# Kernel optimization log

Hardware: AMD Instinct MI355X
Metric: run time of the kernel (lower is better)

## Reference

```python
import jax, jax.numpy as jnp
import numpy as np

WIN_SIZE = 11
SIGMA = 1.5
DATA_RANGE = 1.0
K1, K2 = 0.01, 0.03


def _gaussian_1d(size=WIN_SIZE, sigma=SIGMA):
    coords = np.arange(size, dtype=np.float32) - (size - 1) / 2.0
    g = np.exp(-(coords ** 2) / (2.0 * sigma ** 2))
    g = g / g.sum()
    return jnp.asarray(g, dtype=jnp.float32)


def _gaussian_blur(x):
    # Separable depthwise Gaussian blur, VALID padding (matches pytorch-msssim).
    B, C, H, W = x.shape
    g = _gaussian_1d().astype(x.dtype)
    kh = jnp.tile(g.reshape(1, 1, WIN_SIZE, 1), (C, 1, 1, 1))
    kw = jnp.tile(g.reshape(1, 1, 1, WIN_SIZE), (C, 1, 1, 1))
    dn = ('NCHW', 'OIHW', 'NCHW')
    x = jax.lax.conv_general_dilated(x, kh, (1, 1), 'VALID',
                                     dimension_numbers=dn, feature_group_count=C)
    x = jax.lax.conv_general_dilated(x, kw, (1, 1), 'VALID',
                                     dimension_numbers=dn, feature_group_count=C)
    return x


def _ssim(X, Y):
    C1 = (K1 * DATA_RANGE) ** 2
    C2 = (K2 * DATA_RANGE) ** 2

    mu1 = _gaussian_blur(X)
    mu2 = _gaussian_blur(Y)
    mu1_sq = mu1 * mu1
    mu2_sq = mu2 * mu2
    mu1_mu2 = mu1 * mu2

    sigma1_sq = _gaussian_blur(X * X) - mu1_sq
    sigma2_sq = _gaussian_blur(Y * Y) - mu2_sq
    sigma12 = _gaussian_blur(X * Y) - mu1_mu2

    cs_map = (2.0 * sigma12 + C2) / (sigma1_sq + sigma2_sq + C2)
    ssim_map = ((2.0 * mu1_mu2 + C1) / (mu1_sq + mu2_sq + C1)) * cs_map

    ssim_per_channel = ssim_map.mean(axis=(2, 3))  # [B, C]
    return ssim_per_channel


def setup_inputs() -> dict:
    key = jax.random.key(0)
    k1, k2 = jax.random.split(key)
    predictions = jax.random.uniform(k1, (32, 3, 512, 512), dtype=jnp.float32)
    labels = jax.random.uniform(k2, (32, 3, 512, 512), dtype=jnp.float32)
    return {"predictions": predictions, "labels": labels}


def reference(predictions, labels):
    ssim_per_channel = _ssim(predictions, labels)
    # nonnegative_ssim=True -> relu; size_average=True -> scalar mean
    ssim_val = jax.nn.relu(ssim_per_channel).mean()
    return 1.0 - ssim_val
```

## Files before the change

### kernel.cpp

```cpp
#include <hip/hip_runtime.h>


#define IMG 512
#define OUT_DIM 502
#define WIN 11
#define BH 32
#define NPHASE (BH + WIN - 1)
#define NPLANES 96

template<int PH>
__device__ __forceinline__ void phase_step(int base, int r0, int c0, int cbase,
                                           const float* __restrict__ Xp,
                                           const float* __restrict__ Yp,
                                           float (&a)[5][2][WIN], float& local) {
    constexpr float G[WIN] = {0.00102838f, 0.00759875f, 0.03600077f, 0.10936071f,
                              0.21300553f, 0.26601172f, 0.21300553f, 0.10936071f,
                              0.03600077f, 0.00759875f, 0.00102838f};
    const int p = base + PH;
    if (p >= NPHASE) return;
    const int rr = min(r0 + p, IMG - 1);
    const float* px = Xp + rr * IMG + cbase;
    const float* py = Yp + rr * IMG + cbase;

    float x[12], y[12];
    #pragma unroll
    for (int i = 0; i < 6; ++i) {
        const float2 xv = *(const float2*)(px + 2 * i);
        const float2 yv = *(const float2*)(py + 2 * i);
        x[2 * i] = xv.x; x[2 * i + 1] = xv.y;
        y[2 * i] = yv.x; y[2 * i + 1] = yv.y;
    }
    float xx[12], yy[12], xy[12];
    #pragma unroll
    for (int i = 0; i < 12; ++i) {
        xx[i] = x[i] * x[i];
        yy[i] = y[i] * y[i];
        xy[i] = x[i] * y[i];
    }

    float h[5][2];
    #pragma unroll
    for (int c = 0; c < 2; ++c) {
        float h0 = 0.f, h1 = 0.f, h2 = 0.f, h3 = 0.f, h4 = 0.f;
        #pragma unroll
        for (int k = 0; k < WIN; ++k) {
            h0 = fmaf(G[k], x[k + c], h0);
            h1 = fmaf(G[k], y[k + c], h1);
            h2 = fmaf(G[k], xx[k + c], h2);
            h3 = fmaf(G[k], yy[k + c], h3);
            h4 = fmaf(G[k], xy[k + c], h4);
        }
        h[0][c] = h0; h[1][c] = h1; h[2][c] = h2; h[3][c] = h3; h[4][c] = h4;
    }

    #pragma unroll
    for (int d = 0; d < WIN; ++d) {
        constexpr int ds = PH;
        const int s = (ds - d + 2 * WIN) % WIN;
        const float w = G[d];
        #pragma unroll
        for (int m = 0; m < 5; ++m)
            #pragma unroll
            for (int c = 0; c < 2; ++c)
                a[m][c][s] = (d == 0) ? (w * h[m][c]) : fmaf(w, h[m][c], a[m][c][s]);
    }

    if (p >= WIN - 1) {
        const int o = r0 + p - (WIN - 1);
        if (o < OUT_DIM && c0 < OUT_DIM) {
            constexpr int se = (PH + 1) % WIN;
            const float C1 = 0.0001f, C2 = 0.0009f;
            #pragma unroll
            for (int c = 0; c < 2; ++c) {
                const float m1 = a[0][c][se], m2 = a[1][c][se];
                const float m1sq = m1 * m1, m2sq = m2 * m2, m12 = m1 * m2;
                const float s1  = a[2][c][se] - m1sq;
                const float s2  = a[3][c][se] - m2sq;
                const float s12 = a[4][c][se] - m12;
                const float num = (2.f * m12 + C1) * (2.f * s12 + C2);
                const float den = (m1sq + m2sq + C1) * (s1 + s2 + C2);
                local += num * __builtin_amdgcn_rcpf(den);
            }
        }
    }
}

__global__ __launch_bounds__(256, 2) void ssim_stream(const float* __restrict__ X,
                                                      const float* __restrict__ Y,
                                                      float* __restrict__ planeSums) {
    const int tid = threadIdx.x;
    const int r0 = blockIdx.x * BH;
    const int plane = blockIdx.y;
    const size_t pbase = (size_t)plane * IMG * IMG;
    const float* Xp = X + pbase;
    const float* Yp = Y + pbase;
    const int c0 = tid << 1;
    const int cbase = min(c0, IMG - 12);

    float a[5][2][WIN];
    float local = 0.f;

    for (int base = 0; base < 44; base += WIN) {
        phase_step<0>(base, r0, c0, cbase, Xp, Yp, a, local);
        phase_step<1>(base, r0, c0, cbase, Xp, Yp, a, local);
        phase_step<2>(base, r0, c0, cbase, Xp, Yp, a, local);
        phase_step<3>(base, r0, c0, cbase, Xp, Yp, a, local);
        phase_step<4>(base, r0, c0, cbase, Xp, Yp, a, local);
        phase_step<5>(base, r0, c0, cbase, Xp, Yp, a, local);
        phase_step<6>(base, r0, c0, cbase, Xp, Yp, a, local);
        phase_step<7>(base, r0, c0, cbase, Xp, Yp, a, local);
        phase_step<8>(base, r0, c0, cbase, Xp, Yp, a, local);
        phase_step<9>(base, r0, c0, cbase, Xp, Yp, a, local);
        phase_step<10>(base, r0, c0, cbase, Xp, Yp, a, local);
    }

    #pragma unroll
    for (int off = 32; off > 0; off >>= 1)
        local += __shfl_down(local, off, 64);
    __shared__ float red[4];
    if ((tid & 63) == 0) red[tid >> 6] = local;
    __syncthreads();
    if (tid == 0)
        atomicAdd(&planeSums[plane], (red[0] + red[1]) + (red[2] + red[3]));
}

__global__ __launch_bounds__(128) void ssim_finalize(const float* __restrict__ planeSums,
                                                     float* __restrict__ out) {
    const int tid = threadIdx.x;
    float v = 0.f;
    if (tid < NPLANES) {
        const float m = planeSums[tid] * (1.0f / (float)(OUT_DIM * OUT_DIM));
        v = fmaxf(m, 0.f);
    }
    #pragma unroll
    for (int off = 32; off > 0; off >>= 1)
        v += __shfl_down(v, off, 64);
    __shared__ float red[2];
    if ((tid & 63) == 0) red[tid >> 6] = v;
    __syncthreads();
    if (tid == 0) out[0] = 1.0f - (red[0] + red[1]) * (1.0f / (float)NPLANES);
}

extern "C" void kernel_launch(void* const* d_in, const int* in_sizes, int n_in,
                              void* d_out, int out_size, void* d_ws, size_t ws_size,
                              hipStream_t stream) {
    const float* X = (const float*)d_in[0];
    const float* Y = (const float*)d_in[1];
    float* out = (float*)d_out;
    float* ws  = (float*)d_ws;

    hipMemsetAsync(ws, 0, NPLANES * sizeof(float), stream);

    dim3 grid((OUT_DIM + BH - 1) / BH, NPLANES);
    ssim_stream<<<grid, 256, 0, stream>>>(X, Y, ws);
    ssim_finalize<<<1, 128, 0, stream>>>(ws, out);
}
```

Baseline: 346.5 us.

## Compute one output column per thread with parity-shifted weights for higher occupancy

```diff
diff --git a/kernel.cpp b/kernel.cpp
--- a/kernel.cpp
+++ b/kernel.cpp
@@ -9,10 +9,11 @@
 #define NPLANES 96
 
 template<int PH>
-__device__ __forceinline__ void phase_step(int base, int r0, int c0, int cbase,
+__device__ __forceinline__ void phase_step(int base, int r0, int c, int cbase,
                                            const float* __restrict__ Xp,
                                            const float* __restrict__ Yp,
-                                           float (&a)[5][2][WIN], float& local) {
+                                           const float (&W)[12],
+                                           float (&a)[5][WIN], float& local) {
     constexpr float G[WIN] = {0.00102838f, 0.00759875f, 0.03600077f, 0.10936071f,
                               0.21300553f, 0.26601172f, 0.21300553f, 0.10936071f,
                               0.03600077f, 0.00759875f, 0.00102838f};
@@ -30,88 +31,86 @@
         x[2 * i] = xv.x; x[2 * i + 1] = xv.y;
         y[2 * i] = yv.x; y[2 * i + 1] = yv.y;
     }
-    float xx[12], yy[12], xy[12];
+
+    float h0 = 0.f, h1 = 0.f, h2 = 0.f, h3 = 0.f, h4 = 0.f;
     #pragma unroll
-    for (int i = 0; i < 12; ++i) {
-        xx[i] = x[i] * x[i];
-        yy[i] = y[i] * y[i];
-        xy[i] = x[i] * y[i];
-    }
-
-    float h[5][2];
-    #pragma unroll
-    for (int c = 0; c < 2; ++c) {
-        float h0 = 0.f, h1 = 0.f, h2 = 0.f, h3 = 0.f, h4 = 0.f;
-        #pragma unroll
-        for (int k = 0; k < WIN; ++k) {
-            h0 = fmaf(G[k], x[k + c], h0);
-            h1 = fmaf(G[k], y[k + c], h1);
-            h2 = fmaf(G[k], xx[k + c], h2);
-            h3 = fmaf(G[k], yy[k + c], h3);
-            h4 = fmaf(G[k], xy[k + c], h4);
-        }
-        h[0][c] = h0; h[1][c] = h1; h[2][c] = h2; h[3][c] = h3; h[4][c] = h4;
+    for (int k = 0; k < 12; ++k) {
+        const float w = W[k];
+        h0 = fmaf(w, x[k], h0);
+        h1 = fmaf(w, y[k], h1);
+        const float xx = x[k] * x[k];
+        h2 = fmaf(w, xx, h2);
+        const float yy = y[k] * y[k];
+        h3 = fmaf(w, yy, h3);
+        const float xy = x[k] * y[k];
+        h4 = fmaf(w, xy, h4);
     }
 
     #pragma unroll
     for (int d = 0; d < WIN; ++d) {
-        constexpr int ds = PH;
-        const int s = (ds - d + 2 * WIN) % WIN;
-        const float w = G[d];
-        #pragma unroll
-        for (int m = 0; m < 5; ++m)
-            #pragma unroll
-            for (int c = 0; c < 2; ++c)
-                a[m][c][s] = (d == 0) ? (w * h[m][c]) : fmaf(w, h[m][c], a[m][c][s]);
+        const int s = (PH - d + 2 * WIN) % WIN;
+        const float g = G[d];
+        a[0][s] = (d == 0) ? (g * h0) : fmaf(g, h0, a[0][s]);
+        a[1][s] = (d == 0) ? (g * h1) : fmaf(g, h1, a[1][s]);
+        a[2][s] = (d == 0) ? (g * h2) : fmaf(g, h2, a[2][s]);
+        a[3][s] = (d == 0) ? (g * h3) : fmaf(g, h3, a[3][s]);
+        a[4][s] = (d == 0) ? (g * h4) : fmaf(g, h4, a[4][s]);
     }
 
     if (p >= WIN - 1) {
         const int o = r0 + p - (WIN - 1);
-        if (o < OUT_DIM && c0 < OUT_DIM) {
+        if (o < OUT_DIM && c < OUT_DIM) {
             constexpr int se = (PH + 1) % WIN;
             const float C1 = 0.0001f, C2 = 0.0009f;
-            #pragma unroll
-            for (int c = 0; c < 2; ++c) {
-                const float m1 = a[0][c][se], m2 = a[1][c][se];
-                const float m1sq = m1 * m1, m2sq = m2 * m2, m12 = m1 * m2;
-                const float s1  = a[2][c][se] - m1sq;
-                const float s2  = a[3][c][se] - m2sq;
-                const float s12 = a[4][c][se] - m12;
-                const float num = (2.f * m12 + C1) * (2.f * s12 + C2);
-                const float den = (m1sq + m2sq + C1) * (s1 + s2 + C2);
-                local += num * __builtin_amdgcn_rcpf(den);
-            }
+            const float m1 = a[0][se], m2 = a[1][se];
+            const float m1sq = m1 * m1, m2sq = m2 * m2, m12 = m1 * m2;
+            const float s1  = a[2][se] - m1sq;
+            const float s2  = a[3][se] - m2sq;
+            const float s12 = a[4][se] - m12;
+            const float num = (2.f * m12 + C1) * (2.f * s12 + C2);
+            const float den = (m1sq + m2sq + C1) * (s1 + s2 + C2);
+            local += num * __builtin_amdgcn_rcpf(den);
         }
     }
 }
 
-__global__ __launch_bounds__(256, 2) void ssim_stream(const float* __restrict__ X,
+__global__ __launch_bounds__(256, 4) void ssim_stream(const float* __restrict__ X,
                                                       const float* __restrict__ Y,
                                                       float* __restrict__ planeSums) {
+    constexpr float G[WIN] = {0.00102838f, 0.00759875f, 0.03600077f, 0.10936071f,
+                              0.21300553f, 0.26601172f, 0.21300553f, 0.10936071f,
+                              0.03600077f, 0.00759875f, 0.00102838f};
     const int tid = threadIdx.x;
     const int r0 = blockIdx.x * BH;
-    const int plane = blockIdx.y;
+    const int c = (blockIdx.y << 8) + tid;
+    const int plane = blockIdx.z;
     const size_t pbase = (size_t)plane * IMG * IMG;
     const float* Xp = X + pbase;
     const float* Yp = Y + pbase;
-    const int c0 = tid << 1;
-    const int cbase = min(c0, IMG - 12);
+    const int cbase = min(c & ~1, IMG - 12);
 
-    float a[5][2][WIN];
+    float W[12];
+    const bool odd = (c & 1) != 0;
+    W[0] = odd ? 0.f : G[0];
+    #pragma unroll
+    for (int k = 1; k < 11; ++k) W[k] = odd ? G[k - 1] : G[k];
+    W[11] = odd ? G[10] : 0.f;
+
+    float a[5][WIN];
     float local = 0.f;
 
     for (int base = 0; base < 44; base += WIN) {
-        phase_step<0>(base, r0, c0, cbase, Xp, Yp, a, local);
-        phase_step<1>(base, r0, c0, cbase, Xp, Yp, a, local);
-        phase_step<2>(base, r0, c0, cbase, Xp, Yp, a, local);
-        phase_step<3>(base, r0, c0, cbase, Xp, Yp, a, local);
-        phase_step<4>(base, r0, c0, cbase, Xp, Yp, a, local);
-        phase_step<5>(base, r0, c0, cbase, Xp, Yp, a, local);
-        phase_step<6>(base, r0, c0, cbase, Xp, Yp, a, local);
-        phase_step<7>(base, r0, c0, cbase, Xp, Yp, a, local);
-        phase_step<8>(base, r0, c0, cbase, Xp, Yp, a, local);
-        phase_step<9>(base, r0, c0, cbase, Xp, Yp, a, local);
-        phase_step<10>(base, r0, c0, cbase, Xp, Yp, a, local);
+        phase_step<0>(base, r0, c, cbase, Xp, Yp, W, a, local);
+        phase_step<1>(base, r0, c, cbase, Xp, Yp, W, a, local);
+        phase_step<2>(base, r0, c, cbase, Xp, Yp, W, a, local);
+        phase_step<3>(base, r0, c, cbase, Xp, Yp, W, a, local);
+        phase_step<4>(base, r0, c, cbase, Xp, Yp, W, a, local);
+        phase_step<5>(base, r0, c, cbase, Xp, Yp, W, a, local);
+        phase_step<6>(base, r0, c, cbase, Xp, Yp, W, a, local);
+        phase_step<7>(base, r0, c, cbase, Xp, Yp, W, a, local);
+        phase_step<8>(base, r0, c, cbase, Xp, Yp, W, a, local);
+        phase_step<9>(base, r0, c, cbase, Xp, Yp, W, a, local);
+        phase_step<10>(base, r0, c, cbase, Xp, Yp, W, a, local);
     }
 
     #pragma unroll
@@ -151,7 +150,7 @@
 
     hipMemsetAsync(ws, 0, NPLANES * sizeof(float), stream);
 
-    dim3 grid((OUT_DIM + BH - 1) / BH, NPLANES);
+    dim3 grid((OUT_DIM + BH - 1) / BH, 2, NPLANES);
     ssim_stream<<<grid, 256, 0, stream>>>(X, Y, ws);
     ssim_finalize<<<1, 128, 0, stream>>>(ws, out);
 }
```

New measurement: 333.4 us. 3.8% less time.
